# Kernel optimization log

Measured on AMD Instinct MI355X. Metric: run time of the kernel, lower is better.

## Reference

```python
import jax, jax.numpy as jnp
import numpy as np

B, LB, LC, H = 8, 512, 128, 256
H2 = 2 * H
MIN_WS, N_WIN = 5, 4


def _highway(x, Wn, bn, Wl, bl, Wg, bg):
    # AllenNLP-style highway: per layer, gate * relu(nonlinear) + (1-gate) * linear
    # Wn/Wl/Wg: [L, D, D]; bn/bl/bg: [L, D]
    for i in range(Wn.shape[0]):
        g = jax.nn.sigmoid(x @ Wg[i] + bg[i])
        x = g * jax.nn.relu(x @ Wn[i] + bn[i]) + (1.0 - g) * (x @ Wl[i] + bl[i])
    return x


def _additive_scores(q, k, Wq, bq, Wk, v):
    # 'BilinearAttention' in the repo is additive: v^T tanh(Wq q + Wk k)
    # q: [..., Lq, D], k: [..., Lk, D] -> scores [..., Lq, Lk]
    wq = q @ Wq + bq
    uh = k @ Wk
    return jnp.tanh(wq[..., :, None, :] + uh[..., None, :, :]) @ v


def setup_inputs() -> dict:
    key = jax.random.key(0)
    ks = jax.random.split(key, 32)
    s2 = 1.0 / np.sqrt(H2)
    s1 = 1.0 / np.sqrt(H)
    d = {
        'b_enc_output': jax.random.normal(ks[0], (B, LB, H), jnp.float32),
        'c_enc_output': jax.random.normal(ks[1], (B, LC, H), jnp.float32),
        'c_state': jax.random.normal(ks[2], (B, 1, H), jnp.float32),
        'b_mask': jnp.ones((B, LB), bool),
        'c_mask': jnp.ones((B, LC), bool),
    }
    # b_highway / c_highway: 2 layers, each with nonlinear/linear/gate Linear(2H,2H)
    for pfx, base in (('bh', 3), ('ch', 9)):
        d[pfx + '_Wn'] = jax.random.normal(ks[base + 0], (2, H2, H2), jnp.float32) * s2
        d[pfx + '_bn'] = jnp.zeros((2, H2), jnp.float32)
        d[pfx + '_Wl'] = jax.random.normal(ks[base + 1], (2, H2, H2), jnp.float32) * s2
        d[pfx + '_bl'] = jnp.zeros((2, H2), jnp.float32)
        d[pfx + '_Wg'] = jax.random.normal(ks[base + 2], (2, H2, H2), jnp.float32) * s2
        d[pfx + '_bg'] = jnp.zeros((2, H2), jnp.float32)
    # match_attn (2H) and area_attn (H)
    d['m_Wq'] = jax.random.normal(ks[15], (H2, H2), jnp.float32) * s2
    d['m_bq'] = jnp.zeros((H2,), jnp.float32)
    d['m_Wk'] = jax.random.normal(ks[16], (H2, H2), jnp.float32) * s2
    d['m_v'] = jax.random.normal(ks[17], (H2,), jnp.float32) * s2
    d['a_Wq'] = jax.random.normal(ks[18], (H, H), jnp.float32) * s1
    d['a_bq'] = jnp.zeros((H,), jnp.float32)
    d['a_Wk'] = jax.random.normal(ks[19], (H, H), jnp.float32) * s1
    d['a_v'] = jax.random.normal(ks[20], (H,), jnp.float32) * s1
    return d


def reference(b_enc_output, c_enc_output, c_state,
              bh_Wn, bh_bn, bh_Wl, bh_bl, bh_Wg, bh_bg,
              ch_Wn, ch_bn, ch_Wl, ch_bl, ch_Wg, ch_bg,
              m_Wq, m_bq, m_Wk, m_v,
              a_Wq, a_bq, a_Wk, a_v,
              b_mask, c_mask):
    Bsz, Lb, Hd = b_enc_output.shape
    Lc = c_enc_output.shape[1]
    # match(): highway over [enc ; c_state]
    cs_b = jnp.broadcast_to(c_state, (Bsz, Lb, Hd))
    cs_c = jnp.broadcast_to(c_state, (Bsz, Lc, Hd))
    b = _highway(jnp.concatenate([b_enc_output, cs_b], -1), bh_Wn, bh_bn, bh_Wl, bh_bl, bh_Wg, bh_bg)
    c = _highway(jnp.concatenate([c_enc_output, cs_c], -1), ch_Wn, ch_bn, ch_Wl, ch_bl, ch_Wg, ch_bg)
    m = _additive_scores(b, c, m_Wq, m_bq, m_Wk, m_v)  # [B,Lb,Lc]
    m = jnp.where(c_mask[:, None, :], m, -jnp.inf)
    b_score = jnp.where(b_mask, jnp.max(m, axis=-1), 0.0)  # [B,Lb]
    # segments(): multi-scale sliding windows (unfold) + area attention
    q = c_state[:, :, None, :]  # [B,1,1,H]
    segs, scores = [], []
    for i in range(N_WIN):
        ws = MIN_WS * (i + 1)
        n_seg = (Lb - ws) // MIN_WS + 1
        idx = jnp.arange(n_seg)[:, None] * MIN_WS + jnp.arange(ws)[None, :]  # [n_seg, ws]
        bw = b_enc_output[:, idx, :]  # [B,n_seg,ws,H]
        attn = jax.nn.softmax(_additive_scores(q, bw, a_Wq, a_bq, a_Wk, a_v), axis=-1)  # [B,n_seg,1,ws]
        segs.append(jnp.einsum('bnqw,bnwh->bnh', attn, bw))
        scores.append(b_score[:, idx].sum(-1))  # [B,n_seg]
    segments = jnp.concatenate(segs, axis=1)          # [B,N,H]
    s_score = jax.nn.softmax(jnp.concatenate(scores, axis=1), axis=-1)  # [B,N]
    out = jnp.einsum('bn,bnh->bh', s_score, segments)[:, None, :]  # [B,1,H]
    return out, s_score, b_score
```

## Files before the change

### kernel.cpp

```cpp
#include <hip/hip_runtime.h>
#include <hip/hip_bf16.h>
#include <cstdint>
#include <cstddef>


typedef unsigned short ushort8 __attribute__((ext_vector_type(8)));
typedef float f32x4 __attribute__((ext_vector_type(4)));
typedef float f32x2 __attribute__((ext_vector_type(2)));

__device__ __forceinline__ float fsigmoid(float x) { return 1.0f / (1.0f + __expf(-x)); }
__device__ __forceinline__ float ftanh(float x) {
  float e = __expf(2.0f * x);
  return 1.0f - 2.0f / (e + 1.0f);
}
__device__ __forceinline__ unsigned short f2bf(float x) {
  union { float f; unsigned u; } v; v.f = x;
  unsigned r = (v.u + 0x7FFFu + ((v.u >> 16) & 1u)) >> 16;
  return (unsigned short)r;
}
__device__ __forceinline__ f32x4 mfma_bf16(ushort8 a, ushort8 b, f32x4 c) {
  asm("v_mfma_f32_16x16x32_bf16 %0, %1, %2, %0" : "+v"(c) : "v"(a), "v"(b));
  return c;
}

struct WArg { const float* s[15]; };
__global__ __launch_bounds__(256) void prep_k(WArg wa, unsigned short* __restrict__ WT,
    const float* __restrict__ benc, const float* __restrict__ cenc,
    const float* __restrict__ cs,
    unsigned short* __restrict__ XB0, unsigned short* __restrict__ XC0,
    const float* __restrict__ aWq, const float* __restrict__ abq,
    float* __restrict__ wqa) {
  __shared__ float tile[64][65];
  const int blk = blockIdx.x, t = threadIdx.x;
  if (blk < 960) {
    const int mat = blk >> 6, q = blk & 63;
    const int Kd = (mat == 14) ? 256 : 512;
    const int k0 = (q >> 3) << 6, n0 = (q & 7) << 6;
    if (mat == 14 && (k0 >= 256 || n0 >= 256)) return;
    const float* __restrict__ S = wa.s[mat];
    unsigned short* __restrict__ D = WT + (size_t)mat * 262144;
#pragma unroll
    for (int i = 0; i < 16; ++i) {
      int id = i * 256 + t, r = id >> 6, c = id & 63;
      tile[r][c] = S[(size_t)(k0 + r) * Kd + (n0 + c)];
    }
    __syncthreads();
#pragma unroll
    for (int i = 0; i < 16; ++i) {
      int id = i * 256 + t, r = id >> 6, c = id & 63;
      D[(size_t)(n0 + r) * Kd + (k0 + c)] = f2bf(tile[c][r]);
    }
  } else if (blk < 3520) {
    const bool isB = blk < 3008;
    const float* enc = isB ? benc : cenc;
    unsigned short* out = isB ? XB0 : XC0;
    const int Lshift = isB ? 9 : 7;
    int i4 = (blk - (isB ? 960 : 3008)) * 256 + t;
    int row = i4 >> 7, c4 = (i4 & 127) << 2;
    float4 v;
    if (c4 < 256) v = *(const float4*)(enc + ((size_t)row << 8) + c4);
    else          v = *(const float4*)(cs + ((size_t)(row >> Lshift) << 8) + (c4 - 256));
    union { unsigned short u[4]; uint2 w; } o;
    o.u[0] = f2bf(v.x); o.u[1] = f2bf(v.y); o.u[2] = f2bf(v.z); o.u[3] = f2bf(v.w);
    *(uint2*)(out + ((size_t)row << 9) + c4) = o.w;
  } else {
    int b = blk - 3520, h = t;
    float acc = abq[h];
    for (int k = 0; k < 256; ++k) acc += cs[b * 256 + k] * aWq[k * 256 + h];
    wqa[b * 256 + h] = acc;
  }
}

struct GJob {
  const unsigned short* A; const unsigned short* W0;
  const unsigned short* W1; const unsigned short* W2;
  const float* B0; const float* B1; const float* B2;
  void* Y; int lda, N, K, nbxs , epi, nb, blk0;
};

template <int NB>
__device__ __forceinline__ void gemm_body(const GJob& j, int bx, int by,
                                          unsigned short* sm, int t) {
  const int m0 = by * 64, n0 = bx * 64;
  const int lane = t & 63, wid = t >> 6;
  const int wr = wid >> 1, wc = wid & 1;
  const int N = j.N, K = j.K, lda = j.lda;

  const int srow = t >> 3;
  const int cg = (t & 7) ^ (srow & 7);
  const unsigned short* Ag0 = j.A + (size_t)(m0 + srow) * lda + cg * 8;
  const unsigned short* Ag1 = j.A + (size_t)(m0 + 32 + srow) * lda + cg * 8;
  const unsigned short* Wp[3] = {j.W0, j.W1, j.W2};
  const unsigned short* Bg0[NB], * Bg1[NB];
#pragma unroll
  for (int p = 0; p < NB; ++p) {
    Bg0[p] = Wp[p] + (size_t)(n0 + srow) * K + cg * 8;
    Bg1[p] = Wp[p] + (size_t)(n0 + 32 + srow) * K + cg * 8;
  }
  const int d0 = t * 8, d1 = (256 + t) * 8;

  const int fl = lane & 15, lg = lane >> 4;
  int offA[2][2], offB[2][2];
#pragma unroll
  for (int f = 0; f < 2; ++f) {
    int ra = wr * 32 + f * 16 + fl;
    int rb = wc * 32 + f * 16 + fl;
#pragma unroll
    for (int ks = 0; ks < 2; ++ks) {
      offA[f][ks] = ra * 64 + ((((ks << 2) + lg) ^ (ra & 7)) << 3);
      offB[f][ks] = rb * 64 + ((((ks << 2) + lg) ^ (rb & 7)) << 3);
    }
  }

  f32x4 acc[NB][2][2];
#pragma unroll
  for (int p = 0; p < NB; ++p)
#pragma unroll
    for (int i = 0; i < 2; ++i)
#pragma unroll
      for (int q = 0; q < 2; ++q) acc[p][i][q] = (f32x4){0.f, 0.f, 0.f, 0.f};

  ushort8 ra0 = *(const ushort8*)Ag0, ra1 = *(const ushort8*)Ag1;
  ushort8 rb0[NB], rb1[NB];
#pragma unroll
  for (int p = 0; p < NB; ++p) { rb0[p] = *(const ushort8*)Bg0[p]; rb1[p] = *(const ushort8*)Bg1[p]; }

  for (int k0 = 0; k0 < K; k0 += 64) {
    __syncthreads();
    *(ushort8*)&sm[d0] = ra0;
    *(ushort8*)&sm[d1] = ra1;
#pragma unroll
    for (int p = 0; p < NB; ++p) {
      unsigned short* Bs = sm + (1 + p) * 4096;
      *(ushort8*)&Bs[d0] = rb0[p];
      *(ushort8*)&Bs[d1] = rb1[p];
    }
    __syncthreads();
    if (k0 + 64 < K) {
      ra0 = *(const ushort8*)(Ag0 + k0 + 64);
      ra1 = *(const ushort8*)(Ag1 + k0 + 64);
#pragma unroll
      for (int p = 0; p < NB; ++p) {
        rb0[p] = *(const ushort8*)(Bg0[p] + k0 + 64);
        rb1[p] = *(const ushort8*)(Bg1[p] + k0 + 64);
      }
    }
#pragma unroll
    for (int ks = 0; ks < 2; ++ks) {
      ushort8 a0 = *(const ushort8*)&sm[offA[0][ks]];
      ushort8 a1 = *(const ushort8*)&sm[offA[1][ks]];
#pragma unroll
      for (int p = 0; p < NB; ++p) {
        const unsigned short* Bs = sm + (1 + p) * 4096;
        ushort8 b0 = *(const ushort8*)&Bs[offB[0][ks]];
        ushort8 b1 = *(const ushort8*)&Bs[offB[1][ks]];
        acc[p][0][0] = mfma_bf16(a0, b0, acc[p][0][0]);
        acc[p][0][1] = mfma_bf16(a0, b1, acc[p][0][1]);
        acc[p][1][0] = mfma_bf16(a1, b0, acc[p][1][0]);
        acc[p][1][1] = mfma_bf16(a1, b1, acc[p][1][1]);
      }
    }
  }
  asm volatile("s_nop 7\n\ts_nop 7" ::);

#pragma unroll
  for (int mf = 0; mf < 2; ++mf) {
#pragma unroll
    for (int nf = 0; nf < 2; ++nf) {
      const int col = n0 + wc * 32 + nf * 16 + fl;
      const int row0 = m0 + wr * 32 + mf * 16 + lg * 4;
      if constexpr (NB == 3) {
        float bn = j.B0[col], bl = j.B1[col], bg = j.B2[col];
        unsigned short* Y = (unsigned short*)j.Y;
#pragma unroll
        for (int e = 0; e < 4; ++e) {
          float nv = acc[0][mf][nf][e] + bn;
          float lv = acc[1][mf][nf][e] + bl;
          float gv = fsigmoid(acc[2][mf][nf][e] + bg);
          Y[(size_t)(row0 + e) * N + col] = f2bf(gv * fmaxf(nv, 0.f) + (1.f - gv) * lv);
        }
      } else {
        float* Y = (float*)j.Y;
        if (j.epi == 2) {
          float bb = j.B0[col];
#pragma unroll
          for (int e = 0; e < 4; ++e)
            Y[(size_t)(row0 + e) * N + col] = __expf(2.0f * (acc[0][mf][nf][e] + bb));
        } else if (j.epi == 3) {
          f32x4 w;
#pragma unroll
          for (int e = 0; e < 4; ++e) w[e] = __expf(2.0f * acc[0][mf][nf][e]);
          *(f32x4*)(Y + (((size_t)(row0 >> 7)) << 16) + ((size_t)col << 7) + (row0 & 127)) = w;
        } else {
          float bb = j.B0 ? j.B0[col] : 0.f;
#pragma unroll
          for (int e = 0; e < 4; ++e)
            Y[(size_t)(row0 + e) * N + col] = acc[0][mf][nf][e] + bb;
        }
      }
    }
  }
}

__global__ __launch_bounds__(256) void mgemm3_k(GJob j0, GJob j1, GJob j2, int toff,
    const float* __restrict__ uha, const float* __restrict__ wqa,
    const float* __restrict__ av, float* __restrict__ tout) {
  __shared__ unsigned short sm[4 * 4096];
  const int blk = blockIdx.x, t = threadIdx.x;
  if (blk >= toff) {
    const int lane = t & 63, wid = t >> 6;
    const int pos = (blk - toff) * 4 + wid;
    const int b = pos >> 9;
    const int h0 = lane << 2;
    float4 u = *(const float4*)(uha + (size_t)pos * 256 + h0);
    float4 w = *(const float4*)(wqa + b * 256 + h0);
    float4 v = *(const float4*)(av + h0);
    float s = ftanh(w.x + u.x) * v.x + ftanh(w.y + u.y) * v.y +
              ftanh(w.z + u.z) * v.z + ftanh(w.w + u.w) * v.w;
#pragma unroll
    for (int off = 32; off; off >>= 1) s += __shfl_xor(s, off);
    if (lane == 0) tout[pos] = s;
    return;
  }
  GJob j = j0;
  if (blk >= j1.blk0) j = j1;
  if (blk >= j2.blk0) j = j2;
  const int rel = blk - j.blk0;
  const int bx = rel & ((1 << j.nbxs) - 1), by = rel >> j.nbxs;
  if (j.nb == 3) gemm_body<3>(j, bx, by, sm, t);
  else          gemm_body<1>(j, bx, by, sm, t);
}

__global__ __launch_bounds__(512) void mscore_k(const float* __restrict__ EW,
                                                const float* __restrict__ UHT,
                                                const float* __restrict__ mv,
                                                float* __restrict__ bscore) {
  __shared__ float smem[8 * 512 + 512];
  const int t = threadIdx.x, lane = t & 63, w = t >> 6;
  const int rq = w & 1, hq = w >> 1;
  const int blk = blockIdx.x;
  const int row0 = __builtin_amdgcn_readfirstlane(blk * 8);
  const int b = row0 >> 9;
  const float* __restrict__ up = UHT + ((size_t)b << 16) + ((size_t)(hq * 128) << 7) + (lane << 1);

#pragma unroll
  for (int q = 0; q < 2; ++q) {
    int f4 = q * 512 + t, r = f4 >> 7, c4 = (f4 & 127) << 2;
    *(float4*)&smem[r * 512 + c4] = *(const float4*)(EW + (((size_t)(row0 + r)) << 9) + c4);
  }
  if (t < 128) *(float4*)&smem[4096 + (t << 2)] = *(const float4*)(mv + (t << 2));
  __syncthreads();

  const float* __restrict__ eb = &smem[(rq * 4) * 512 + hq * 128];
  const float* __restrict__ vb = &smem[4096 + hq * 128];

  f32x2 acc0 = {0.f, 0.f}, acc1 = {0.f, 0.f}, acc2 = {0.f, 0.f}, acc3 = {0.f, 0.f};
  f32x2 uA[4], uB[4];

#define LOADU(U, h0_)                                                      \
  { _Pragma("unroll") for (int hh = 0; hh < 4; ++hh)                       \
      U[hh] = *(const f32x2*)(up + ((size_t)((h0_) + hh) << 7)); }
#define COMPB(U, h0_)                                                      \
  {                                                                        \
    f32x4 e0 = *(const f32x4*)(eb + 0 * 512 + (h0_));                      \
    f32x4 e1 = *(const f32x4*)(eb + 1 * 512 + (h0_));                      \
    f32x4 e2 = *(const f32x4*)(eb + 2 * 512 + (h0_));                      \
    f32x4 e3 = *(const f32x4*)(eb + 3 * 512 + (h0_));                      \
    f32x4 v4 = *(const f32x4*)(vb + (h0_));                                \
    _Pragma("unroll") for (int hh = 0; hh < 4; ++hh) {                     \
      float vvv = v4[hh];                                                  \
      f32x2 u = U[hh];                                                     \
      acc0.x += vvv * __builtin_amdgcn_rcpf(__builtin_fmaf(e0[hh], u.x, 1.f)); \
      acc0.y += vvv * __builtin_amdgcn_rcpf(__builtin_fmaf(e0[hh], u.y, 1.f)); \
      acc1.x += vvv * __builtin_amdgcn_rcpf(__builtin_fmaf(e1[hh], u.x, 1.f)); \
      acc1.y += vvv * __builtin_amdgcn_rcpf(__builtin_fmaf(e1[hh], u.y, 1.f)); \
      acc2.x += vvv * __builtin_amdgcn_rcpf(__builtin_fmaf(e2[hh], u.x, 1.f)); \
      acc2.y += vvv * __builtin_amdgcn_rcpf(__builtin_fmaf(e2[hh], u.y, 1.f)); \
      acc3.x += vvv * __builtin_amdgcn_rcpf(__builtin_fmaf(e3[hh], u.x, 1.f)); \
      acc3.y += vvv * __builtin_amdgcn_rcpf(__builtin_fmaf(e3[hh], u.y, 1.f)); \
    }                                                                      \
  }

  LOADU(uA, 0)
#pragma unroll
  for (int i = 0; i < 32; i += 2) {
    LOADU(uB, (i + 1) * 4)
    COMPB(uA, i * 4)
    if (i + 2 < 32) LOADU(uA, (i + 2) * 4)
    COMPB(uB, (i + 1) * 4)
  }
#undef LOADU
#undef COMPB

  __syncthreads();
  float* part = smem;
  {
    const int base = ((rq * 4 + hq) * 4) * 128 + (lane << 1);
    *(f32x2*)&part[base + 0 * 128] = acc0;
    *(f32x2*)&part[base + 1 * 128] = acc1;
    *(f32x2*)&part[base + 2 * 128] = acc2;
    *(f32x2*)&part[base + 3 * 128] = acc3;
  }
  __syncthreads();

  if (w < 2) {
    float V = 0.f;
#pragma unroll
    for (int k = 0; k < 8; ++k) V += smem[4096 + lane + (k << 6)];
#pragma unroll
    for (int off = 32; off; off >>= 1) V += __shfl_xor(V, off);

    float mr[4];
#pragma unroll
    for (int r = 0; r < 4; ++r) {
      f32x2 s0 = *(const f32x2*)&part[((w * 4 + 0) * 4 + r) * 128 + (lane << 1)];
      f32x2 s1 = *(const f32x2*)&part[((w * 4 + 1) * 4 + r) * 128 + (lane << 1)];
      f32x2 s2 = *(const f32x2*)&part[((w * 4 + 2) * 4 + r) * 128 + (lane << 1)];
      f32x2 s3 = *(const f32x2*)&part[((w * 4 + 3) * 4 + r) * 128 + (lane << 1)];
      float sx = s0.x + s1.x + s2.x + s3.x;
      float sy = s0.y + s1.y + s2.y + s3.y;
      mr[r] = fminf(sx, sy);
    }
#pragma unroll
    for (int off = 32; off; off >>= 1) {
#pragma unroll
      for (int r = 0; r < 4; ++r) mr[r] = fminf(mr[r], __shfl_xor(mr[r], off));
    }
    if (lane == 0) {
      const int ro = blk * 8 + w * 4;
#pragma unroll
      for (int r = 0; r < 4; ++r) bscore[ro + r] = V - 2.f * mr[r];
    }
  }
}

__global__ __launch_bounds__(256) void seg_k(const float* __restrict__ t,
                                             const float* __restrict__ bscore,
                                             const float* __restrict__ benc,
                                             float* __restrict__ seg,
                                             float* __restrict__ sco) {
  const int s = blockIdx.x, b = blockIdx.y, h = threadIdx.x;
  int i, n;
  if (s < 102)      { i = 0; n = s; }
  else if (s < 203) { i = 1; n = s - 102; }
  else if (s < 303) { i = 2; n = s - 203; }
  else              { i = 3; n = s - 303; }
  const int ws = 5 * (i + 1), start = n * 5;
  const float* tb = t + b * 512 + start;
  float mx = -3.0e38f;
  for (int w = 0; w < ws; ++w) mx = fmaxf(mx, tb[w]);
  float sum = 0.f;
  for (int w = 0; w < ws; ++w) sum += __expf(tb[w] - mx);
  float inv = 1.f / sum;
  float acc = 0.f;
  for (int w = 0; w < ws; ++w)
    acc += __expf(tb[w] - mx) * benc[((size_t)(b * 512 + start + w)) * 256 + h];
  seg[((size_t)(b * 402 + s)) * 256 + h] = acc * inv;
  if (h == 0) {
    float ss = 0.f;
    const float* bs = bscore + b * 512 + start;
    for (int w = 0; w < ws; ++w) ss += bs[w];
    sco[b * 402 + s] = ss;
  }
}

__global__ __launch_bounds__(256) void final_k(const float* __restrict__ sco,
                                               const float* __restrict__ seg,
                                               float* __restrict__ dout) {
  const int b = blockIdx.x, tid = threadIdx.x, lane = tid & 63, wid = tid >> 6;
  __shared__ float sc[402];
  __shared__ float redm[4], reds[4];
  for (int s = tid; s < 402; s += 256) sc[s] = sco[b * 402 + s];
  __syncthreads();
  float m = -3.0e38f;
  for (int s = tid; s < 402; s += 256) m = fmaxf(m, sc[s]);
#pragma unroll
  for (int off = 32; off; off >>= 1) m = fmaxf(m, __shfl_xor(m, off));
  if (lane == 0) redm[wid] = m;
  __syncthreads();
  m = fmaxf(fmaxf(redm[0], redm[1]), fmaxf(redm[2], redm[3]));
  float p = 0.f;
  for (int s = tid; s < 402; s += 256) p += __expf(sc[s] - m);
#pragma unroll
  for (int off = 32; off; off >>= 1) p += __shfl_xor(p, off);
  if (lane == 0) reds[wid] = p;
  __syncthreads();
  float invS = 1.f / (reds[0] + reds[1] + reds[2] + reds[3]);
  for (int s = tid; s < 402; s += 256) {
    float pv = __expf(sc[s] - m) * invS;
    dout[2048 + b * 402 + s] = pv;
    sc[s] = pv;
  }
  __syncthreads();
  float acc = 0.f;
  for (int s = 0; s < 402; ++s)
    acc += sc[s] * seg[((size_t)(b * 402 + s)) * 256 + tid];
  dout[b * 256 + tid] = acc;
}

extern "C" void kernel_launch(void* const* d_in, const int* in_sizes, int n_in,
                              void* d_out, int out_size, void* d_ws, size_t ws_size,
                              hipStream_t stream) {
  const float* b_enc   = (const float*)d_in[0];
  const float* c_enc   = (const float*)d_in[1];
  const float* c_state = (const float*)d_in[2];
  const float* bh_Wn = (const float*)d_in[5];
  const float* bh_bn = (const float*)d_in[6];
  const float* bh_Wl = (const float*)d_in[7];
  const float* bh_bl = (const float*)d_in[8];
  const float* bh_Wg = (const float*)d_in[9];
  const float* bh_bg = (const float*)d_in[10];
  const float* ch_Wn = (const float*)d_in[11];
  const float* ch_bn = (const float*)d_in[12];
  const float* ch_Wl = (const float*)d_in[13];
  const float* ch_bl = (const float*)d_in[14];
  const float* ch_Wg = (const float*)d_in[15];
  const float* ch_bg = (const float*)d_in[16];
  const float* m_Wq  = (const float*)d_in[17];
  const float* m_bq  = (const float*)d_in[18];
  const float* m_Wk  = (const float*)d_in[19];
  const float* m_v   = (const float*)d_in[20];
  const float* a_Wq  = (const float*)d_in[21];
  const float* a_bq  = (const float*)d_in[22];
  const float* a_Wk  = (const float*)d_in[23];
  const float* a_v   = (const float*)d_in[24];

  uint8_t* base = (uint8_t*)d_ws;
  unsigned short* WT  = (unsigned short*)(base);
  unsigned short* WTa = WT + 14 * 262144;
  unsigned short* XB0 = (unsigned short*)(base + 7471104);
  unsigned short* XB1 = (unsigned short*)(base + 11665408);
  unsigned short* XC0 = (unsigned short*)(base + 15859712);
  unsigned short* XC1 = (unsigned short*)(base + 16908288);
  float* EW   = (float*)(base + 17956864);
  float* UHT  = (float*)(base + 26345472);
  float* UHA  = (float*)(base + 28442624);
  float* WQA  = (float*)(base + 32636928);
  float* T    = (float*)(base + 32645120);
  float* SEG  = (float*)(base + 32661504);
  float* SCO  = (float*)(base + 35954688);

  float* out = (float*)d_out;
  float* BSC = out + 5264;

  const int S = 262144;
  const int LW = 262144;
  const int SENT = 1 << 30;

  WArg wa;
  wa.s[0] = bh_Wn; wa.s[1] = bh_Wn + LW;
  wa.s[2] = bh_Wl; wa.s[3] = bh_Wl + LW;
  wa.s[4] = bh_Wg; wa.s[5] = bh_Wg + LW;
  wa.s[6] = ch_Wn; wa.s[7] = ch_Wn + LW;
  wa.s[8] = ch_Wl; wa.s[9] = ch_Wl + LW;
  wa.s[10] = ch_Wg; wa.s[11] = ch_Wg + LW;
  wa.s[12] = m_Wq; wa.s[13] = m_Wk; wa.s[14] = a_Wk;

  prep_k<<<3528, 256, 0, stream>>>(wa, WT, b_enc, c_enc, c_state, XB0, XC0,
                                   a_Wq, a_bq, WQA);

  {
    GJob jb = {XB0, WT, WT + 2 * S, WT + 4 * S, bh_bn, bh_bl, bh_bg,
               XB1, 512, 512, 512, 3, 1, 3, 0};
    GJob jc = {XC0, WT + 6 * S, WT + 8 * S, WT + 10 * S, ch_bn, ch_bl, ch_bg,
               XC1, 512, 512, 512, 3, 1, 3, 512};
    GJob ja = {XB0, WTa, nullptr, nullptr, nullptr, nullptr, nullptr,
               UHA, 512, 256, 256, 2, 0, 1, 640};
    mgemm3_k<<<896, 256, 0, stream>>>(jb, jc, ja, 896, nullptr, nullptr, nullptr, nullptr);
  }
  {
    GJob jb = {XB1, WT + S, WT + 3 * S, WT + 5 * S, bh_bn + 512, bh_bl + 512, bh_bg + 512,
               XB0, 512, 512, 512, 3, 1, 3, 0};
    GJob jc = {XC1, WT + 7 * S, WT + 9 * S, WT + 11 * S, ch_bn + 512, ch_bl + 512, ch_bg + 512,
               XC0, 512, 512, 512, 3, 1, 3, 512};
    GJob js = jc; js.blk0 = SENT;
    mgemm3_k<<<640, 256, 0, stream>>>(jb, jc, js, 640, nullptr, nullptr, nullptr, nullptr);
  }
  {
    GJob je = {XB0, WT + 12 * S, nullptr, nullptr, m_bq, nullptr, nullptr,
               EW, 512, 512, 512, 3, 2, 1, 0};
    GJob ju = {XC0, WT + 13 * S, nullptr, nullptr, nullptr, nullptr, nullptr,
               UHT, 512, 512, 512, 3, 3, 1, 512};
    GJob js = ju; js.blk0 = SENT;
    mgemm3_k<<<1664, 256, 0, stream>>>(je, ju, js, 640, UHA, WQA, a_v, T);
  }

  mscore_k<<<512, 512, 0, stream>>>(EW, UHT, m_v, BSC);
  seg_k<<<dim3(402, 8), 256, 0, stream>>>(T, BSC, b_enc, SEG, SCO);
  final_k<<<8, 256, 0, stream>>>(SCO, SEG, out);
}
```

Measured before the change: 137.8 us.

## Fold area-attention and segment pooling into GEMM launches, drop seg kernel

The area-attention tanh scoring moves into the second highway GEMM launch as extra blocks. The segment softmax pooling moves into the EW/UHT GEMM launch as extra blocks, and window score sums move into final_k, which removes the separate seg_k launch and the SCO buffer. mscore_k is restructured to 256 threads per block with 4 rows per block (1024 blocks) and each wave owning a quarter of H. The intent is fewer launches and better overlap of small work with GEMM tails, at the cost of more divergent block roles inside one kernel.

```diff
diff --git a/kernel.cpp b/kernel.cpp
--- a/kernel.cpp
+++ b/kernel.cpp
@@ -7,6 +7,8 @@
 typedef unsigned short ushort8 __attribute__((ext_vector_type(8)));
 typedef float f32x4 __attribute__((ext_vector_type(4)));
 typedef float f32x2 __attribute__((ext_vector_type(2)));
+
+#define SS 262144
 
 __device__ __forceinline__ float fsigmoid(float x) { return 1.0f / (1.0f + __expf(-x)); }
 __device__ __forceinline__ float ftanh(float x) {
@@ -38,7 +40,7 @@
     const int k0 = (q >> 3) << 6, n0 = (q & 7) << 6;
     if (mat == 14 && (k0 >= 256 || n0 >= 256)) return;
     const float* __restrict__ S = wa.s[mat];
-    unsigned short* __restrict__ D = WT + (size_t)mat * 262144;
+    unsigned short* __restrict__ D = WT + (size_t)mat * SS;
 #pragma unroll
     for (int i = 0; i < 16; ++i) {
       int id = i * 256 + t, r = id >> 6, c = id & 63;
@@ -104,11 +106,11 @@
 #pragma unroll
   for (int f = 0; f < 2; ++f) {
     int ra = wr * 32 + f * 16 + fl;
-    int rb = wc * 32 + f * 16 + fl;
+    int rb2 = wc * 32 + f * 16 + fl;
 #pragma unroll
     for (int ks = 0; ks < 2; ++ks) {
       offA[f][ks] = ra * 64 + ((((ks << 2) + lg) ^ (ra & 7)) << 3);
-      offB[f][ks] = rb * 64 + ((((ks << 2) + lg) ^ (rb & 7)) << 3);
+      offB[f][ks] = rb2 * 64 + ((((ks << 2) + lg) ^ (rb2 & 7)) << 3);
     }
   }
 
@@ -202,24 +204,49 @@
   }
 }
 
-__global__ __launch_bounds__(256) void mgemm3_k(GJob j0, GJob j1, GJob j2, int toff,
-    const float* __restrict__ uha, const float* __restrict__ wqa,
-    const float* __restrict__ av, float* __restrict__ tout) {
+__global__ __launch_bounds__(256) void mgemm3_k(GJob j0, GJob j1, GJob j2,
+    int toff, int tmode,
+    const float* __restrict__ p0,
+    const float* __restrict__ p1,
+    const float* __restrict__ p2,
+    float* __restrict__ pout) {
   __shared__ unsigned short sm[4 * 4096];
   const int blk = blockIdx.x, t = threadIdx.x;
   if (blk >= toff) {
-    const int lane = t & 63, wid = t >> 6;
-    const int pos = (blk - toff) * 4 + wid;
-    const int b = pos >> 9;
-    const int h0 = lane << 2;
-    float4 u = *(const float4*)(uha + (size_t)pos * 256 + h0);
-    float4 w = *(const float4*)(wqa + b * 256 + h0);
-    float4 v = *(const float4*)(av + h0);
-    float s = ftanh(w.x + u.x) * v.x + ftanh(w.y + u.y) * v.y +
-              ftanh(w.z + u.z) * v.z + ftanh(w.w + u.w) * v.w;
-#pragma unroll
-    for (int off = 32; off; off >>= 1) s += __shfl_xor(s, off);
-    if (lane == 0) tout[pos] = s;
+    const int rel = blk - toff;
+    if (tmode == 1) {
+      const int lane = t & 63, wid = t >> 6;
+      const int pos = (rel << 2) + wid;
+      const int b = pos >> 9;
+      const int h0 = lane << 2;
+      float4 u = *(const float4*)(p0 + (size_t)pos * 256 + h0);
+      float4 w = *(const float4*)(p1 + b * 256 + h0);
+      float4 v = *(const float4*)(p2 + h0);
+      float s = ftanh(w.x + u.x) * v.x + ftanh(w.y + u.y) * v.y +
+                ftanh(w.z + u.z) * v.z + ftanh(w.w + u.w) * v.w;
+#pragma unroll
+      for (int off = 32; off; off >>= 1) s += __shfl_xor(s, off);
+      if (lane == 0) pout[pos] = s;
+    } else {
+      const int b = rel / 402, s = rel - b * 402;
+      const int h = t;
+      int i, n;
+      if (s < 102)      { i = 0; n = s; }
+      else if (s < 203) { i = 1; n = s - 102; }
+      else if (s < 303) { i = 2; n = s - 203; }
+      else              { i = 3; n = s - 303; }
+      const int ws = 5 * (i + 1), start = n * 5;
+      const float* tb = p0 + b * 512 + start;
+      float mx = -3.0e38f;
+      for (int w = 0; w < ws; ++w) mx = fmaxf(mx, tb[w]);
+      float sum = 0.f;
+      for (int w = 0; w < ws; ++w) sum += __expf(tb[w] - mx);
+      float inv = 1.f / sum;
+      float acc = 0.f;
+      for (int w = 0; w < ws; ++w)
+        acc += __expf(tb[w] - mx) * p1[((size_t)(b * 512 + start + w)) * 256 + h];
+      pout[((size_t)(b * 402 + s)) * 256 + h] = acc * inv;
+    }
     return;
   }
   GJob j = j0;
@@ -231,162 +258,136 @@
   else          gemm_body<1>(j, bx, by, sm, t);
 }
 
-__global__ __launch_bounds__(512) void mscore_k(const float* __restrict__ EW,
+__device__ __forceinline__ void ms_comp(const float* eb, const float* vbp, int h0,
+    f32x2 u0, f32x2 u1, f32x2 u2, f32x2 u3,
+    f32x2& a0, f32x2& a1, f32x2& a2, f32x2& a3) {
+  f32x4 v4 = *(const f32x4*)(vbp + h0);
+#pragma unroll
+  for (int r = 0; r < 4; ++r) {
+    f32x2& ar = (r == 0) ? a0 : (r == 1) ? a1 : (r == 2) ? a2 : a3;
+    f32x4 e4 = *(const f32x4*)(eb + r * 512 + h0);
+    ar.x = __builtin_fmaf(v4[0], __builtin_amdgcn_rcpf(__builtin_fmaf(e4[0], u0.x, 1.f)), ar.x);
+    ar.y = __builtin_fmaf(v4[0], __builtin_amdgcn_rcpf(__builtin_fmaf(e4[0], u0.y, 1.f)), ar.y);
+    ar.x = __builtin_fmaf(v4[1], __builtin_amdgcn_rcpf(__builtin_fmaf(e4[1], u1.x, 1.f)), ar.x);
+    ar.y = __builtin_fmaf(v4[1], __builtin_amdgcn_rcpf(__builtin_fmaf(e4[1], u1.y, 1.f)), ar.y);
+    ar.x = __builtin_fmaf(v4[2], __builtin_amdgcn_rcpf(__builtin_fmaf(e4[2], u2.x, 1.f)), ar.x);
+    ar.y = __builtin_fmaf(v4[2], __builtin_amdgcn_rcpf(__builtin_fmaf(e4[2], u2.y, 1.f)), ar.y);
+    ar.x = __builtin_fmaf(v4[3], __builtin_amdgcn_rcpf(__builtin_fmaf(e4[3], u3.x, 1.f)), ar.x);
+    ar.y = __builtin_fmaf(v4[3], __builtin_amdgcn_rcpf(__builtin_fmaf(e4[3], u3.y, 1.f)), ar.y);
+  }
+}
+
+__global__ __launch_bounds__(256) void mscore_k(const float* __restrict__ EW,
                                                 const float* __restrict__ UHT,
                                                 const float* __restrict__ mv,
                                                 float* __restrict__ bscore) {
-  __shared__ float smem[8 * 512 + 512];
+  __shared__ __align__(16) float smem[4 * 512 + 512];
+  float* ews = smem;
+  float* vvs = smem + 2048;
   const int t = threadIdx.x, lane = t & 63, w = t >> 6;
-  const int rq = w & 1, hq = w >> 1;
-  const int blk = blockIdx.x;
-  const int row0 = __builtin_amdgcn_readfirstlane(blk * 8);
+  const int vb = blockIdx.x;
+  const int row0 = vb << 2;
   const int b = row0 >> 9;
-  const float* __restrict__ up = UHT + ((size_t)b << 16) + ((size_t)(hq * 128) << 7) + (lane << 1);
-
 #pragma unroll
   for (int q = 0; q < 2; ++q) {
-    int f4 = q * 512 + t, r = f4 >> 7, c4 = (f4 & 127) << 2;
-    *(float4*)&smem[r * 512 + c4] = *(const float4*)(EW + (((size_t)(row0 + r)) << 9) + c4);
-  }
-  if (t < 128) *(float4*)&smem[4096 + (t << 2)] = *(const float4*)(mv + (t << 2));
-  __syncthreads();
-
-  const float* __restrict__ eb = &smem[(rq * 4) * 512 + hq * 128];
-  const float* __restrict__ vb = &smem[4096 + hq * 128];
-
-  f32x2 acc0 = {0.f, 0.f}, acc1 = {0.f, 0.f}, acc2 = {0.f, 0.f}, acc3 = {0.f, 0.f};
-  f32x2 uA[4], uB[4];
-
-#define LOADU(U, h0_)                                                      \
-  { _Pragma("unroll") for (int hh = 0; hh < 4; ++hh)                       \
-      U[hh] = *(const f32x2*)(up + ((size_t)((h0_) + hh) << 7)); }
-#define COMPB(U, h0_)                                                      \
-  {                                                                        \
-    f32x4 e0 = *(const f32x4*)(eb + 0 * 512 + (h0_));                      \
-    f32x4 e1 = *(const f32x4*)(eb + 1 * 512 + (h0_));                      \
-    f32x4 e2 = *(const f32x4*)(eb + 2 * 512 + (h0_));                      \
-    f32x4 e3 = *(const f32x4*)(eb + 3 * 512 + (h0_));                      \
-    f32x4 v4 = *(const f32x4*)(vb + (h0_));                                \
-    _Pragma("unroll") for (int hh = 0; hh < 4; ++hh) {                     \
-      float vvv = v4[hh];                                                  \
-      f32x2 u = U[hh];                                                     \
-      acc0.x += vvv * __builtin_amdgcn_rcpf(__builtin_fmaf(e0[hh], u.x, 1.f)); \
-      acc0.y += vvv * __builtin_amdgcn_rcpf(__builtin_fmaf(e0[hh], u.y, 1.f)); \
-      acc1.x += vvv * __builtin_amdgcn_rcpf(__builtin_fmaf(e1[hh], u.x, 1.f)); \
-      acc1.y += vvv * __builtin_amdgcn_rcpf(__builtin_fmaf(e1[hh], u.y, 1.f)); \
-      acc2.x += vvv * __builtin_amdgcn_rcpf(__builtin_fmaf(e2[hh], u.x, 1.f)); \
-      acc2.y += vvv * __builtin_amdgcn_rcpf(__builtin_fmaf(e2[hh], u.y, 1.f)); \
-      acc3.x += vvv * __builtin_amdgcn_rcpf(__builtin_fmaf(e3[hh], u.x, 1.f)); \
-      acc3.y += vvv * __builtin_amdgcn_rcpf(__builtin_fmaf(e3[hh], u.y, 1.f)); \
-    }                                                                      \
-  }
-
-  LOADU(uA, 0)
+    int f4 = q * 256 + t, r = f4 >> 7, c4 = (f4 & 127) << 2;
+    *(float4*)&ews[r * 512 + c4] =
+        *(const float4*)(EW + (((size_t)(row0 + r)) << 9) + c4);
+  }
+  if (t < 128) *(float4*)&vvs[t << 2] = *(const float4*)(mv + (t << 2));
+  __syncthreads();
+
+  const float* up = UHT + ((size_t)b << 16) + (w << 14) + (lane << 1);
+  const float* eb = ews + (w << 7);
+  const float* vbp = vvs + (w << 7);
+
+  f32x2 a0 = {0.f, 0.f}, a1 = {0.f, 0.f}, a2 = {0.f, 0.f}, a3 = {0.f, 0.f};
+  f32x2 uA0, uA1, uA2, uA3, uB0, uB1, uB2, uB3;
+  uA0 = *(const f32x2*)(up + 0 * 128);
+  uA1 = *(const f32x2*)(up + 1 * 128);
+  uA2 = *(const f32x2*)(up + 2 * 128);
+  uA3 = *(const f32x2*)(up + 3 * 128);
 #pragma unroll
   for (int i = 0; i < 32; i += 2) {
-    LOADU(uB, (i + 1) * 4)
-    COMPB(uA, i * 4)
-    if (i + 2 < 32) LOADU(uA, (i + 2) * 4)
-    COMPB(uB, (i + 1) * 4)
-  }
-#undef LOADU
-#undef COMPB
+    const int hB = (i + 1) * 4, hN = (i + 2) * 4;
+    uB0 = *(const f32x2*)(up + (size_t)(hB + 0) * 128);
+    uB1 = *(const f32x2*)(up + (size_t)(hB + 1) * 128);
+    uB2 = *(const f32x2*)(up + (size_t)(hB + 2) * 128);
+    uB3 = *(const f32x2*)(up + (size_t)(hB + 3) * 128);
+    ms_comp(eb, vbp, i * 4, uA0, uA1, uA2, uA3, a0, a1, a2, a3);
+    if (i + 2 < 32) {
+      uA0 = *(const f32x2*)(up + (size_t)(hN + 0) * 128);
+      uA1 = *(const f32x2*)(up + (size_t)(hN + 1) * 128);
+      uA2 = *(const f32x2*)(up + (size_t)(hN + 2) * 128);
+      uA3 = *(const f32x2*)(up + (size_t)(hN + 3) * 128);
+    }
+    ms_comp(eb, vbp, hB, uB0, uB1, uB2, uB3, a0, a1, a2, a3);
+  }
 
   __syncthreads();
   float* part = smem;
+  *(f32x2*)&part[((w * 4 + 0) * 128) + (lane << 1)] = a0;
+  *(f32x2*)&part[((w * 4 + 1) * 128) + (lane << 1)] = a1;
+  *(f32x2*)&part[((w * 4 + 2) * 128) + (lane << 1)] = a2;
+  *(f32x2*)&part[((w * 4 + 3) * 128) + (lane << 1)] = a3;
+  __syncthreads();
+
   {
-    const int base = ((rq * 4 + hq) * 4) * 128 + (lane << 1);
-    *(f32x2*)&part[base + 0 * 128] = acc0;
-    *(f32x2*)&part[base + 1 * 128] = acc1;
-    *(f32x2*)&part[base + 2 * 128] = acc2;
-    *(f32x2*)&part[base + 3 * 128] = acc3;
-  }
-  __syncthreads();
-
-  if (w < 2) {
+    const int r = w;
+    f32x2 s0 = *(const f32x2*)&part[((0 * 4 + r) * 128) + (lane << 1)];
+    f32x2 s1 = *(const f32x2*)&part[((1 * 4 + r) * 128) + (lane << 1)];
+    f32x2 s2 = *(const f32x2*)&part[((2 * 4 + r) * 128) + (lane << 1)];
+    f32x2 s3 = *(const f32x2*)&part[((3 * 4 + r) * 128) + (lane << 1)];
+    float sx = s0.x + s1.x + s2.x + s3.x;
+    float sy = s0.y + s1.y + s2.y + s3.y;
+    float m = fminf(sx, sy);
+#pragma unroll
+    for (int off = 32; off; off >>= 1) m = fminf(m, __shfl_xor(m, off));
     float V = 0.f;
 #pragma unroll
-    for (int k = 0; k < 8; ++k) V += smem[4096 + lane + (k << 6)];
+    for (int k = 0; k < 8; ++k) V += vvs[lane + (k << 6)];
 #pragma unroll
     for (int off = 32; off; off >>= 1) V += __shfl_xor(V, off);
-
-    float mr[4];
-#pragma unroll
-    for (int r = 0; r < 4; ++r) {
-      f32x2 s0 = *(const f32x2*)&part[((w * 4 + 0) * 4 + r) * 128 + (lane << 1)];
-      f32x2 s1 = *(const f32x2*)&part[((w * 4 + 1) * 4 + r) * 128 + (lane << 1)];
-      f32x2 s2 = *(const f32x2*)&part[((w * 4 + 2) * 4 + r) * 128 + (lane << 1)];
-      f32x2 s3 = *(const f32x2*)&part[((w * 4 + 3) * 4 + r) * 128 + (lane << 1)];
-      float sx = s0.x + s1.x + s2.x + s3.x;
-      float sy = s0.y + s1.y + s2.y + s3.y;
-      mr[r] = fminf(sx, sy);
-    }
-#pragma unroll
-    for (int off = 32; off; off >>= 1) {
-#pragma unroll
-      for (int r = 0; r < 4; ++r) mr[r] = fminf(mr[r], __shfl_xor(mr[r], off));
-    }
-    if (lane == 0) {
-      const int ro = blk * 8 + w * 4;
-#pragma unroll
-      for (int r = 0; r < 4; ++r) bscore[ro + r] = V - 2.f * mr[r];
-    }
-  }
-}
-
-__global__ __launch_bounds__(256) void seg_k(const float* __restrict__ t,
-                                             const float* __restrict__ bscore,
-                                             const float* __restrict__ benc,
-                                             float* __restrict__ seg,
-                                             float* __restrict__ sco) {
-  const int s = blockIdx.x, b = blockIdx.y, h = threadIdx.x;
-  int i, n;
-  if (s < 102)      { i = 0; n = s; }
-  else if (s < 203) { i = 1; n = s - 102; }
-  else if (s < 303) { i = 2; n = s - 203; }
-  else              { i = 3; n = s - 303; }
-  const int ws = 5 * (i + 1), start = n * 5;
-  const float* tb = t + b * 512 + start;
-  float mx = -3.0e38f;
-  for (int w = 0; w < ws; ++w) mx = fmaxf(mx, tb[w]);
-  float sum = 0.f;
-  for (int w = 0; w < ws; ++w) sum += __expf(tb[w] - mx);
-  float inv = 1.f / sum;
-  float acc = 0.f;
-  for (int w = 0; w < ws; ++w)
-    acc += __expf(tb[w] - mx) * benc[((size_t)(b * 512 + start + w)) * 256 + h];
-  seg[((size_t)(b * 402 + s)) * 256 + h] = acc * inv;
-  if (h == 0) {
-    float ss = 0.f;
-    const float* bs = bscore + b * 512 + start;
-    for (int w = 0; w < ws; ++w) ss += bs[w];
-    sco[b * 402 + s] = ss;
-  }
-}
-
-__global__ __launch_bounds__(256) void final_k(const float* __restrict__ sco,
+    if (lane == 0) bscore[row0 + r] = V - 2.f * m;
+  }
+}
+
+__global__ __launch_bounds__(256) void final_k(const float* __restrict__ bscore,
                                                const float* __restrict__ seg,
                                                float* __restrict__ dout) {
-  const int b = blockIdx.x, tid = threadIdx.x, lane = tid & 63, wid = tid >> 6;
+  const int b = blockIdx.x, t = threadIdx.x, lane = t & 63, wid = t >> 6;
   __shared__ float sc[402];
+  __shared__ float bsc[512];
   __shared__ float redm[4], reds[4];
-  for (int s = tid; s < 402; s += 256) sc[s] = sco[b * 402 + s];
+  for (int i = t; i < 512; i += 256) bsc[i] = bscore[b * 512 + i];
+  __syncthreads();
+  for (int s = t; s < 402; s += 256) {
+    int i, n;
+    if (s < 102)      { i = 0; n = s; }
+    else if (s < 203) { i = 1; n = s - 102; }
+    else if (s < 303) { i = 2; n = s - 203; }
+    else              { i = 3; n = s - 303; }
+    const int ws = 5 * (i + 1), start = n * 5;
+    float ss = 0.f;
+    for (int w = 0; w < ws; ++w) ss += bsc[start + w];
+    sc[s] = ss;
+  }
   __syncthreads();
   float m = -3.0e38f;
-  for (int s = tid; s < 402; s += 256) m = fmaxf(m, sc[s]);
+  for (int s = t; s < 402; s += 256) m = fmaxf(m, sc[s]);
 #pragma unroll
   for (int off = 32; off; off >>= 1) m = fmaxf(m, __shfl_xor(m, off));
   if (lane == 0) redm[wid] = m;
   __syncthreads();
   m = fmaxf(fmaxf(redm[0], redm[1]), fmaxf(redm[2], redm[3]));
   float p = 0.f;
-  for (int s = tid; s < 402; s += 256) p += __expf(sc[s] - m);
+  for (int s = t; s < 402; s += 256) p += __expf(sc[s] - m);
 #pragma unroll
   for (int off = 32; off; off >>= 1) p += __shfl_xor(p, off);
   if (lane == 0) reds[wid] = p;
   __syncthreads();
   float invS = 1.f / (reds[0] + reds[1] + reds[2] + reds[3]);
-  for (int s = tid; s < 402; s += 256) {
+  for (int s = t; s < 402; s += 256) {
     float pv = __expf(sc[s] - m) * invS;
     dout[2048 + b * 402 + s] = pv;
     sc[s] = pv;
@@ -394,8 +395,8 @@
   __syncthreads();
   float acc = 0.f;
   for (int s = 0; s < 402; ++s)
-    acc += sc[s] * seg[((size_t)(b * 402 + s)) * 256 + tid];
-  dout[b * 256 + tid] = acc;
+    acc += sc[s] * seg[((size_t)(b * 402 + s)) * 256 + t];
+  dout[b * 256 + t] = acc;
 }
 
 extern "C" void kernel_launch(void* const* d_in, const int* in_sizes, int n_in,
@@ -427,7 +428,7 @@
 
   uint8_t* base = (uint8_t*)d_ws;
   unsigned short* WT  = (unsigned short*)(base);
-  unsigned short* WTa = WT + 14 * 262144;
+  unsigned short* WTa = WT + 14 * SS;
   unsigned short* XB0 = (unsigned short*)(base + 7471104);
   unsigned short* XB1 = (unsigned short*)(base + 11665408);
   unsigned short* XC0 = (unsigned short*)(base + 15859712);
@@ -438,12 +439,10 @@
   float* WQA  = (float*)(base + 32636928);
   float* T    = (float*)(base + 32645120);
   float* SEG  = (float*)(base + 32661504);
-  float* SCO  = (float*)(base + 35954688);
 
   float* out = (float*)d_out;
   float* BSC = out + 5264;
 
-  const int S = 262144;
   const int LW = 262144;
   const int SENT = 1 << 30;
 
@@ -460,32 +459,31 @@
                                    a_Wq, a_bq, WQA);
 
   {
-    GJob jb = {XB0, WT, WT + 2 * S, WT + 4 * S, bh_bn, bh_bl, bh_bg,
+    GJob jb = {XB0, WT, WT + 2 * SS, WT + 4 * SS, bh_bn, bh_bl, bh_bg,
                XB1, 512, 512, 512, 3, 1, 3, 0};
-    GJob jc = {XC0, WT + 6 * S, WT + 8 * S, WT + 10 * S, ch_bn, ch_bl, ch_bg,
+    GJob jc = {XC0, WT + 6 * SS, WT + 8 * SS, WT + 10 * SS, ch_bn, ch_bl, ch_bg,
                XC1, 512, 512, 512, 3, 1, 3, 512};
     GJob ja = {XB0, WTa, nullptr, nullptr, nullptr, nullptr, nullptr,
                UHA, 512, 256, 256, 2, 0, 1, 640};
-    mgemm3_k<<<896, 256, 0, stream>>>(jb, jc, ja, 896, nullptr, nullptr, nullptr, nullptr);
+    mgemm3_k<<<896, 256, 0, stream>>>(jb, jc, ja, 896, 0,
+                                      nullptr, nullptr, nullptr, nullptr);
   }
   {
-    GJob jb = {XB1, WT + S, WT + 3 * S, WT + 5 * S, bh_bn + 512, bh_bl + 512, bh_bg + 512,
-               XB0, 512, 512, 512, 3, 1, 3, 0};
-    GJob jc = {XC1, WT + 7 * S, WT + 9 * S, WT + 11 * S, ch_bn + 512, ch_bl + 512, ch_bg + 512,
-               XC0, 512, 512, 512, 3, 1, 3, 512};
+    GJob jb = {XB1, WT + SS, WT + 3 * SS, WT + 5 * SS,
+               bh_bn + 512, bh_bl + 512, bh_bg + 512, XB0, 512, 512, 512, 3, 1, 3, 0};
+    GJob jc = {XC1, WT + 7 * SS, WT + 9 * SS, WT + 11 * SS,
+               ch_bn + 512, ch_bl + 512, ch_bg + 512, XC0, 512, 512, 512, 3, 1, 3, 512};
     GJob js = jc; js.blk0 = SENT;
-    mgemm3_k<<<640, 256, 0, stream>>>(jb, jc, js, 640, nullptr, nullptr, nullptr, nullptr);
+    mgemm3_k<<<1664, 256, 0, stream>>>(jb, jc, js, 640, 1, UHA, WQA, a_v, T);
   }
   {
-    GJob je = {XB0, WT + 12 * S, nullptr, nullptr, m_bq, nullptr, nullptr,
+    GJob je = {XB0, WT + 12 * SS, nullptr, nullptr, m_bq, nullptr, nullptr,
                EW, 512, 512, 512, 3, 2, 1, 0};
-    GJob ju = {XC0, WT + 13 * S, nullptr, nullptr, nullptr, nullptr, nullptr,
+    GJob ju = {XC0, WT + 13 * SS, nullptr, nullptr, nullptr, nullptr, nullptr,
                UHT, 512, 512, 512, 3, 3, 1, 512};
     GJob js = ju; js.blk0 = SENT;
-    mgemm3_k<<<1664, 256, 0, stream>>>(je, ju, js, 640, UHA, WQA, a_v, T);
-  }
-
-  mscore_k<<<512, 512, 0, stream>>>(EW, UHT, m_v, BSC);
-  seg_k<<<dim3(402, 8), 256, 0, stream>>>(T, BSC, b_enc, SEG, SCO);
-  final_k<<<8, 256, 0, stream>>>(SCO, SEG, out);
-}
+    mgemm3_k<<<3856, 256, 0, stream>>>(je, ju, js, 640, 2, T, b_enc, nullptr, SEG);
+  }
+  mscore_k<<<1024, 256, 0, stream>>>(EW, UHT, m_v, BSC);
+  final_k<<<8, 256, 0, stream>>>(BSC, SEG, out);
+}
```

After: 140.3 us. Within noise of the previous version (+1.8%).
